# Kernel tuning notes

Measured on AMD Instinct MI355X. Metric: run time of the kernel, lower is better.

## Reference

```python
import jax, jax.numpy as jnp
import numpy as np
import math


def hs_pe(x, fr, fi):
    # x: [N, c, h, w], c = cp*3; fr/fi: [max_len, cp] real/imag of freqs_cis.
    N, c, h, w = x.shape
    cp = c // 3
    xs = x.reshape(N, cp, 3, h, w)
    a, b, c3 = xs[:, :, 0], xs[:, :, 1], xs[:, :, 2]
    # rotate (a, b) as complex along h axis
    frh = fr[:h].T[None, :, :, None]  # [1, cp, h, 1]
    fih = fi[:h].T[None, :, :, None]
    a2 = a * frh - b * fih
    b2 = a * fih + b * frh
    # rotate (b2, c3) as complex along w axis
    frw = fr[:w].T[None, :, None, :]  # [1, cp, 1, w]
    fiw = fi[:w].T[None, :, None, :]
    b3 = b2 * frw - c3 * fiw
    c32 = b2 * fiw + c3 * frw
    return jnp.stack([a2, b3, c32], axis=2).reshape(N, c, h, w)


def partition(x, ws, dr):
    # OverlapDilatedWindowPartion
    B, C, H, W = x.shape
    Wsz = ws + dr
    st = Wsz // 2
    nh = math.ceil(H / Wsz)
    nw = math.ceil(W / Wsz)
    x = jnp.pad(x, ((0, 0), (0, 0), (0, nh * Wsz - H), (0, nw * Wsz - W)), mode='reflect')
    x = jnp.concatenate([x, jnp.pad(x[:, :, st:, :], ((0, 0), (0, 0), (0, st), (0, 0)), mode='reflect')], axis=0)
    x = jnp.concatenate([x, jnp.pad(x[:, :, :, st:], ((0, 0), (0, 0), (0, 0), (0, st)), mode='reflect')], axis=0)
    gb = x.shape[0]
    # 'gb c (nh h) (nw w) -> (nh nw gb) c h w'
    x = x.reshape(gb, C, nh, Wsz, nw, Wsz).transpose(2, 4, 0, 1, 3, 5).reshape(nh * nw * gb, C, Wsz, Wsz)
    return x[:, :, :ws, :ws]


def reverse(win, ws, dr, B, H, W):
    # OverlapDilatedWindowReverse
    Wsz = ws + dr
    st = Wsz // 2
    nh = math.ceil(H / Wsz)
    nw = math.ceil(W / Wsz)
    bH, bW = nh * Wsz, nw * Wsz
    win = jnp.pad(win, ((0, 0), (0, 0), (0, dr), (0, dr)))
    C = win.shape[1]
    # '(nh nw g b) c h w -> g b c (nh h) (nw w)'
    x = win.reshape(nh, nw, 4, B, C, Wsz, Wsz).transpose(2, 3, 4, 0, 5, 1, 6).reshape(4, B, C, bH, bW)
    x0 = x[0]
    x1 = jnp.pad(x[1], ((0, 0), (0, 0), (st, 0), (0, 0)))[:, :, :bH, :]
    x2 = jnp.pad(x[2], ((0, 0), (0, 0), (0, 0), (st, 0)))[:, :, :, :bW]
    x3 = jnp.pad(x[3], ((0, 0), (0, 0), (st, 0), (st, 0)))[:, :, :bH, :bW]
    return (x0 + x1 + x2 + x3)[:, :, :H, :W]


HEAD_NUM = 8
WINDOW_SIZE = 8
DILATE_RATE = 4


def setup_inputs() -> dict:
    key = jax.random.key(0)
    k1, k2, k3 = jax.random.split(key, 3)
    B, C, H, W = 1, 576, 192, 192
    x = jax.random.normal(k1, (B, C, H, W), dtype=jnp.float32)
    # rotary frequencies on the unit circle: [window_size, d//3, 2] (real, imag)
    theta = jax.random.uniform(k2, (WINDOW_SIZE, C // (3 * HEAD_NUM) // 3), dtype=jnp.float32) * (2 * np.pi)
    freqs_cis = jnp.stack([jnp.cos(theta), jnp.sin(theta)], axis=-1)
    weight = jax.random.uniform(k3, (1, 1, H, W), dtype=jnp.float32, minval=0.5, maxval=1.5)
    return {"x": x, "freqs_cis": freqs_cis, "weight": weight}


def reference(x, freqs_cis, weight):
    B, C, H, W = x.shape
    ws, dr, n = WINDOW_SIZE, DILATE_RATE, HEAD_NUM
    win = partition(x, ws, dr)  # [Nw, C, ws, ws]
    Nw = win.shape[0]
    d = C // (3 * n)
    # '(k n d)' channel split, k outer, d fastest
    qkv = win.reshape(Nw, 3, n, d, ws, ws).transpose(1, 0, 2, 3, 4, 5).reshape(3, Nw * n, d, ws, ws)
    fr, fi = freqs_cis[..., 0], freqs_cis[..., 1]
    q = hs_pe(qkv[0], fr, fi)
    k = hs_pe(qkv[1], fr, fi)
    v = qkv[2]
    def toseq(t):
        return t.reshape(Nw * n, d, ws * ws).transpose(0, 2, 1)  # [Nw*n, L, d]
    q, k, v = toseq(q), toseq(k), toseq(v)
    scale = jnp.sqrt(jnp.asarray(d, q.dtype))
    attn = jax.nn.softmax(jnp.einsum('nld,nmd->nlm', q, k) / scale, axis=-1)
    out = jnp.einsum('nlm,nmd->nld', attn, v)
    # '(Nw n) (h w) d -> Nw (n d) h w'
    out = out.reshape(Nw, n, ws, ws, d).transpose(0, 1, 4, 2, 3).reshape(Nw, n * d, ws, ws)
    out = reverse(out, ws, dr, B, H, W)
    return out / weight
```

## Files before the change

### kernel.cpp

```cpp
#include <hip/hip_runtime.h>

#define HW 36864
#define HDIM 192
#define NUNITS 8192
#define UPB 2
#define UDW 2688
#define QO 0
#define KO 768
#define VTO 1536
#define PO 0
#define P_BYTES (384ull * HW * 4)

typedef __fp16 h2  __attribute__((ext_vector_type(2)));
typedef __fp16 v8h __attribute__((ext_vector_type(8)));
typedef float  v4f __attribute__((ext_vector_type(4)));

static __device__ __forceinline__ h2 pk2(float a, float b) {
    return __builtin_amdgcn_cvt_pkrtz(a, b);
}
static __device__ __forceinline__ unsigned h2u(h2 x) {
    union { h2 h; unsigned u; } c; c.h = x; return c.u;
}
static __device__ __forceinline__ h2 u2h(unsigned x) {
    union { unsigned u; h2 h; } c; c.u = x; return c.h;
}
static __device__ __forceinline__ v8h as_v8h(uint4 u) {
    union { uint4 u; v8h h; } c; c.u = u; return c.h;
}

__global__ __launch_bounds__(128, 2)
void attn_mfma(const float* __restrict__ x,
               const float* __restrict__ fc,
               const float* __restrict__ wgt,
               float* __restrict__ out,
               unsigned* __restrict__ wsP)
{
    __shared__ unsigned lds[UPB * UDW];
    __shared__ float frs[64], fis[64];
    __shared__ unsigned zblk[4];

    const int wave = threadIdx.x >> 6;
    const int lane = threadIdx.x & 63;
    const int gid  = blockIdx.x * UPB + wave;
    const int head = gid & 7;
    const int wi   = gid >> 3;
    const int g    = wi & 3;
    const int iw   = (wi >> 2) & 15;
    const int ih   = wi >> 6;

    unsigned* uld = &lds[wave * UDW];

    if (threadIdx.x < 64) {
        float2 t = ((const float2*)fc)[threadIdx.x];
        frs[threadIdx.x] = t.x; fis[threadIdx.x] = t.y;
    } else if (threadIdx.x < 68) {
        zblk[threadIdx.x - 64] = 0;
    }
    __syncthreads();

    const int r = lane >> 3, col = lane & 7;
    const int h0 = ih * 12 + r, w0 = iw * 12 + col;
    int in_h = h0 + ((g & 1) ? 6 : 0); if (in_h >= HDIM) in_h = 2 * HDIM - 2 - in_h;
    int in_w = w0 + ((g & 2) ? 6 : 0); if (in_w >= HDIM) in_w = 2 * HDIM - 2 - in_w;

    float q[24], k[24], v[24];
    {
        const float* xb = x + (size_t)(head * 24) * HW + in_h * HDIM + in_w;
#pragma unroll
        for (int dd = 0; dd < 24; ++dd) q[dd] = xb[(size_t)dd * HW];
#pragma unroll
        for (int dd = 0; dd < 24; ++dd) k[dd] = xb[(size_t)dd * HW + (size_t)192 * HW];
#pragma unroll
        for (int dd = 0; dd < 24; ++dd) v[dd] = xb[(size_t)dd * HW + (size_t)384 * HW];
    }

#pragma unroll
    for (int p = 0; p < 8; ++p) {
        const float frr = frs[r * 8 + p],   fir = fis[r * 8 + p];
        const float frc = frs[col * 8 + p], fic = fis[col * 8 + p];
        {
            float a = q[3*p], b = q[3*p+1], c3 = q[3*p+2];
            float b2 = a * fir + b * frr;
            q[3*p]   = a * frr - b * fir;
            q[3*p+1] = b2 * frc - c3 * fic;
            q[3*p+2] = b2 * fic + c3 * frc;
        }
        {
            float a = k[3*p], b = k[3*p+1], c3 = k[3*p+2];
            float b2 = a * fir + b * frr;
            k[3*p]   = a * frr - b * fir;
            k[3*p+1] = b2 * frc - c3 * fic;
            k[3*p+2] = b2 * fic + c3 * frc;
        }
    }

    {
        const float sc = 0.29448903f;
        uint2* qw = (uint2*)&uld[QO + lane * 12];
        uint2* kw = (uint2*)&uld[KO + lane * 12];
#pragma unroll
        for (int j = 0; j < 3; ++j) {
            qw[2*j]   = make_uint2(h2u(pk2(q[8*j]*sc,   q[8*j+1]*sc)),
                                   h2u(pk2(q[8*j+2]*sc, q[8*j+3]*sc)));
            qw[2*j+1] = make_uint2(h2u(pk2(q[8*j+4]*sc, q[8*j+5]*sc)),
                                   h2u(pk2(q[8*j+6]*sc, q[8*j+7]*sc)));
            kw[2*j]   = make_uint2(h2u(pk2(k[8*j],   k[8*j+1])),
                                   h2u(pk2(k[8*j+2], k[8*j+3])));
            kw[2*j+1] = make_uint2(h2u(pk2(k[8*j+4], k[8*j+5])),
                                   h2u(pk2(k[8*j+6], k[8*j+7])));
        }
    }
    {
#pragma unroll
        for (int i = 0; i < 5; ++i) {
            int idx = lane + i * 64;
            if (idx < 288) uld[VTO + 24 * 36 + idx] = 0;
        }
        __fp16* vt = (__fp16*)&uld[VTO];
        vt[24 * 72 + lane] = (__fp16)1.0f;
#pragma unroll
        for (int dd = 0; dd < 24; ++dd) vt[dd * 72 + lane] = (__fp16)v[dd];
    }
    asm volatile("" ::: "memory");

    const int qq = lane >> 4, l15 = lane & 15;
    v8h Qf[4], Kf[4];
#pragma unroll
    for (int t = 0; t < 4; ++t) {
        const unsigned* qa = (qq < 3) ? &uld[QO + (16*t + l15)*12 + 4*qq] : zblk;
        const unsigned* ka = (qq < 3) ? &uld[KO + (16*t + l15)*12 + 4*qq] : zblk;
        Qf[t] = as_v8h(*(const uint4*)qa);
        Kf[t] = as_v8h(*(const uint4*)ka);
    }
    v8h Vf[2][2];
#pragma unroll
    for (int dt = 0; dt < 2; ++dt)
#pragma unroll
        for (int ks = 0; ks < 2; ++ks)
            Vf[dt][ks] = as_v8h(*(const uint4*)&uld[VTO + (16*dt + l15)*36 + 16*ks + 4*qq]);

#pragma unroll
    for (int tn = 0; tn < 4; ++tn) {
#pragma unroll
        for (int tm = 0; tm < 4; ++tm) {
            v4f c = {0.f, 0.f, 0.f, 0.f};
            c = __builtin_amdgcn_mfma_f32_16x16x32_f16(Kf[tn], Qf[tm], c, 0, 0, 0);
            uint2 w = make_uint2(h2u(pk2(__builtin_amdgcn_exp2f(c[0]),
                                         __builtin_amdgcn_exp2f(c[1]))),
                                 h2u(pk2(__builtin_amdgcn_exp2f(c[2]),
                                         __builtin_amdgcn_exp2f(c[3]))));
            *(uint2*)&uld[PO + (16*tm + l15)*36 + 8*tn + 2*qq] = w;
        }
    }

    v4f O[2][4];
#pragma unroll
    for (int dt = 0; dt < 2; ++dt)
#pragma unroll
        for (int lt = 0; lt < 4; ++lt)
            O[dt][lt] = (v4f){0.f, 0.f, 0.f, 0.f};
#pragma unroll
    for (int lt = 0; lt < 4; ++lt) {
#pragma unroll
        for (int ks = 0; ks < 2; ++ks) {
            v8h Pf = as_v8h(*(const uint4*)&uld[PO + (16*lt + l15)*36 + 16*ks + 4*qq]);
            O[0][lt] = __builtin_amdgcn_mfma_f32_16x16x32_f16(Vf[0][ks], Pf, O[0][lt], 0, 0, 0);
            O[1][lt] = __builtin_amdgcn_mfma_f32_16x16x32_f16(Vf[1][ks], Pf, O[1][lt], 0, 0, 0);
        }
    }

    float inv[4];
#pragma unroll
    for (int lt = 0; lt < 4; ++lt)
        inv[lt] = 1.0f / __shfl(O[1][lt][0], 32 + l15, 64);

    if (wsP) {
        unsigned* sm = uld;
        asm volatile("" ::: "memory");
#pragma unroll
        for (int lt = 0; lt < 4; ++lt) {
            const int   l  = 16*lt + l15;
            const float sc = inv[lt];
            sm[l*12 + 2*qq]     = h2u(pk2(O[0][lt][0]*sc, O[0][lt][1]*sc));
            sm[l*12 + 2*qq + 1] = h2u(pk2(O[0][lt][2]*sc, O[0][lt][3]*sc));
            if (qq < 2) {
                sm[l*12 + 8 + 2*qq] = h2u(pk2(O[1][lt][0]*sc, O[1][lt][1]*sc));
                sm[l*12 + 9 + 2*qq] = h2u(pk2(O[1][lt][2]*sc, O[1][lt][3]*sc));
            }
        }
        asm volatile("" ::: "memory");
        const int goffh = (g & 1) ? 6 : 0, goffw = (g & 2) ? 6 : 0;
        const int oh = ih * 12 + (lane >> 3) + goffh;
        const int ow = iw * 12 + (lane & 7)  + goffw;
        if (oh < HDIM && ow < HDIM) {
            uint4* dst = (uint4*)&wsP[((size_t)(g * 8 + head) * HW
                                       + (size_t)oh * HDIM + ow) * 12];
            const uint4* src = (const uint4*)&sm[lane * 12];
            dst[0] = src[0]; dst[1] = src[1]; dst[2] = src[2];
        }
    } else {
#pragma unroll
        for (int lt = 0; lt < 4; ++lt) {
            const int l  = 16*lt + l15;
            const int oh = ih * 12 + (l >> 3) + ((g & 1) ? 6 : 0);
            const int ow = iw * 12 + (l & 7)  + ((g & 2) ? 6 : 0);
            if (oh < HDIM && ow < HDIM) {
                const float sc = inv[lt] / wgt[oh * HDIM + ow];
                float* ob = out + (size_t)(head * 24) * HW + oh * HDIM + ow;
#pragma unroll
                for (int rg = 0; rg < 4; ++rg)
                    atomicAdd(ob + (size_t)(4*qq + rg) * HW, O[0][lt][rg] * sc);
                if (qq < 2) {
#pragma unroll
                    for (int rg = 0; rg < 4; ++rg)
                        atomicAdd(ob + (size_t)(16 + 4*qq + rg) * HW, O[1][lt][rg] * sc);
                }
            }
        }
    }
}

__global__ __launch_bounds__(256)
void merge_out(const unsigned* __restrict__ wsP,
               const float* __restrict__ wgt,
               float* __restrict__ out)
{
    const int idx  = blockIdx.x * 256 + threadIdx.x;
    const int head = idx / HW;
    const int pix  = idx - head * HW;
    const int h    = pix / HDIM;
    const int w    = pix - h * HDIM;

    float acc[24];
#pragma unroll
    for (int d = 0; d < 24; ++d) acc[d] = 0.f;

#pragma unroll
    for (int g = 0; g < 4; ++g) {
        const int hh = h - ((g & 1) ? 6 : 0);
        const int ww = w - ((g & 2) ? 6 : 0);
        if (hh < 0 || ww < 0) continue;
        if (hh % 12 >= 8 || ww % 12 >= 8) continue;
        const uint4* src = (const uint4*)&wsP[((size_t)(g * 8 + head) * HW + pix) * 12];
#pragma unroll
        for (int j = 0; j < 3; ++j) {
            const uint4 u = src[j];
#pragma unroll
            for (int t = 0; t < 4; ++t) {
                const h2 p = u2h(((const unsigned*)&u)[t]);
                acc[8*j + 2*t]     += (float)p[0];
                acc[8*j + 2*t + 1] += (float)p[1];
            }
        }
    }
    const float wv = wgt[pix];
#pragma unroll
    for (int d = 0; d < 24; ++d)
        out[(size_t)(head * 24 + d) * HW + pix] = acc[d] / wv;
}

extern "C" void kernel_launch(void* const* d_in, const int* in_sizes, int n_in,
                              void* d_out, int out_size, void* d_ws, size_t ws_size,
                              hipStream_t stream) {
    const float* x   = (const float*)d_in[0];
    const float* fc  = (const float*)d_in[1];
    const float* wgt = (const float*)d_in[2];
    float* out = (float*)d_out;

    unsigned* wsP = ws_size >= P_BYTES ? (unsigned*)d_ws : nullptr;

    if (!wsP)
        (void)hipMemsetAsync(out, 0, (size_t)out_size * sizeof(float), stream);
    attn_mfma<<<NUNITS / UPB, UPB * 64, 0, stream>>>(x, fc, wgt, out, wsP);
    if (wsP)
        merge_out<<<8 * HW / 256, 256, 0, stream>>>(wsP, wgt, out);
}
```

Measured before the change: 178.0 us.

## Stage window inputs through LDS with 16-byte loads, one wave per block

Each block now holds a single wave instead of two. In non-reflected windows the 72 channel rows are fetched with coalesced 16-byte vector loads into LDS and then redistributed to per-lane registers, replacing scalar strided 4-byte gathers. Windows that reflect at the right edge keep the old scalar path. The LDS buffer grows to 4608 words per block, and the single-wave blocks change the occupancy and scheduling pattern.

New measurement: 174.0 us. 2.2% less time.

```diff
diff --git a/kernel.cpp b/kernel.cpp
--- a/kernel.cpp
+++ b/kernel.cpp
@@ -3,8 +3,7 @@
 #define HW 36864
 #define HDIM 192
 #define NUNITS 8192
-#define UPB 2
-#define UDW 2688
+#define RDW 4608
 #define QO 0
 #define KO 768
 #define VTO 1536
@@ -28,33 +27,31 @@
     union { uint4 u; v8h h; } c; c.u = u; return c.h;
 }
 
-__global__ __launch_bounds__(128, 2)
+__global__ __launch_bounds__(64)
 void attn_mfma(const float* __restrict__ x,
                const float* __restrict__ fc,
                const float* __restrict__ wgt,
                float* __restrict__ out,
                unsigned* __restrict__ wsP)
 {
-    __shared__ unsigned lds[UPB * UDW];
+    __shared__ unsigned lds[RDW];
     __shared__ float frs[64], fis[64];
     __shared__ unsigned zblk[4];
 
-    const int wave = threadIdx.x >> 6;
-    const int lane = threadIdx.x & 63;
-    const int gid  = blockIdx.x * UPB + wave;
+    const int lane = threadIdx.x;
+    const int gid  = blockIdx.x;
     const int head = gid & 7;
     const int wi   = gid >> 3;
     const int g    = wi & 3;
     const int iw   = (wi >> 2) & 15;
     const int ih   = wi >> 6;
 
-    unsigned* uld = &lds[wave * UDW];
-
-    if (threadIdx.x < 64) {
-        float2 t = ((const float2*)fc)[threadIdx.x];
-        frs[threadIdx.x] = t.x; fis[threadIdx.x] = t.y;
-    } else if (threadIdx.x < 68) {
-        zblk[threadIdx.x - 64] = 0;
+    unsigned* uld = lds;
+
+    {
+        float2 t = ((const float2*)fc)[lane];
+        frs[lane] = t.x; fis[lane] = t.y;
+        if (lane < 4) zblk[lane] = 0;
     }
     __syncthreads();
 
@@ -64,7 +61,32 @@
     int in_w = w0 + ((g & 2) ? 6 : 0); if (in_w >= HDIM) in_w = 2 * HDIM - 2 - in_w;
 
     float q[24], k[24], v[24];
-    {
+    const bool wrefl = (g & 2) && (iw == 15);
+    if (!wrefl) {
+        const int ch4  = lane >> 4;
+        const int row  = (lane & 15) >> 1;
+        const int half = lane & 1;
+        int rh = ih * 12 + row + ((g & 1) ? 6 : 0);
+        if (rh >= HDIM) rh = 2 * HDIM - 2 - rh;
+        const int wb = iw * 12 + ((g & 2) ? 6 : 0);
+        const size_t rowoff = (size_t)rh * HDIM + wb + half * 4;
+        unsigned* dst0 = &lds[ch4 * 64 + row * 8 + half * 4];
+#pragma unroll
+        for (int i = 0; i < 18; ++i) {
+            const int c72 = i * 4 + ch4;
+            const int qkv = c72 / 24, dd = c72 - qkv * 24;
+            const float* src = x + (size_t)(qkv * 192 + head * 24 + dd) * HW + rowoff;
+            *(uint4*)(dst0 + (size_t)i * 256) = *(const uint4*)src;
+        }
+        asm volatile("" ::: "memory");
+        const float* Rf = (const float*)lds;
+#pragma unroll
+        for (int dd = 0; dd < 24; ++dd) q[dd] = Rf[dd * 64 + lane];
+#pragma unroll
+        for (int dd = 0; dd < 24; ++dd) k[dd] = Rf[(24 + dd) * 64 + lane];
+#pragma unroll
+        for (int dd = 0; dd < 24; ++dd) v[dd] = Rf[(48 + dd) * 64 + lane];
+    } else {
         const float* xb = x + (size_t)(head * 24) * HW + in_h * HDIM + in_w;
 #pragma unroll
         for (int dd = 0; dd < 24; ++dd) q[dd] = xb[(size_t)dd * HW];
@@ -94,6 +116,7 @@
         }
     }
 
+    asm volatile("" ::: "memory");
     {
         const float sc = 0.29448903f;
         uint2* qw = (uint2*)&uld[QO + lane * 12];
@@ -271,7 +294,7 @@
 
     if (!wsP)
         (void)hipMemsetAsync(out, 0, (size_t)out_size * sizeof(float), stream);
-    attn_mfma<<<NUNITS / UPB, UPB * 64, 0, stream>>>(x, fc, wgt, out, wsP);
+    attn_mfma<<<NUNITS, 64, 0, stream>>>(x, fc, wgt, out, wsP);
     if (wsP)
         merge_out<<<8 * HW / 256, 256, 0, stream>>>(wsP, wgt, out);
 }
```
